# Performance work log

Hardware: AMD Instinct MI355X
Metric: run time of the kernel (lower is better)

## Reference

```python
import jax, jax.numpy as jnp
import numpy as np

NEWS_DIM = 400
HID = 200  # user_query_vector_dim
B, L0 = 512, 200
MIN_LOG = 2  # min_log_length=1 incremented by add_pad


def setup_inputs() -> dict:
    key = jax.random.key(0)
    k1, k2, k3, k4, k5 = jax.random.split(key, 5)
    log_vec = jax.random.normal(k1, (B, L0, NEWS_DIM), dtype=jnp.float32)
    log_mask = jnp.ones((B, L0), dtype=jnp.float32)
    pad_embedding = jax.random.normal(k2, (1, NEWS_DIM), dtype=jnp.float32)
    # att_fc1: Linear(news_dim -> hid), att_fc2: Linear(hid -> 1)
    W1 = jax.random.normal(k3, (HID, NEWS_DIM), dtype=jnp.float32) / np.sqrt(NEWS_DIM)
    b1 = jnp.zeros((HID,), dtype=jnp.float32)
    W2 = jax.random.normal(k4, (1, HID), dtype=jnp.float32) / np.sqrt(HID)
    b2 = jnp.zeros((1,), dtype=jnp.float32)
    return {"log_vec": log_vec, "log_mask": log_mask, "pad_embedding": pad_embedding,
            "W1": W1, "b1": b1, "W2": W2, "b2": b2}


def reference(log_vec, log_mask, pad_embedding, W1, b1, W2, b2):
    Bz, _, D = log_vec.shape
    # add_pad: prepend pad doc, then drop last -> (B, L, D) with L = L0
    pad = jnp.broadcast_to(pad_embedding, (Bz, 1, D))
    vec = jnp.concatenate([pad, log_vec], axis=1)[:, :-1, :]
    L = vec.shape[1]
    G = L + 1 - MIN_LOG  # = L0 - 1
    # autor_mask = ones(L,G).triu(1-MIN_LOG).T -> (G, L)
    tri = jnp.triu(jnp.ones((L, G), dtype=jnp.float32), k=1 - MIN_LOG).T
    # use_pad=False: multiply in history mask (broadcast over L)
    auto_mask = tri[None, :, :] * log_mask[:, :-1, None]  # (B, G, L)
    # score MLP computed once per (B, L); identical across G so broadcast
    s = (jnp.tanh(jnp.einsum('bld,hd->blh', vec, W1) + b1) @ W2.T + b2)[..., 0]  # (B, L)
    w = jnp.where(auto_mask == 0, jnp.float32(-1e8), s[:, None, :])  # (B, G, L)
    w = jax.nn.softmax(w, axis=-1)
    user_vec = jnp.einsum('bgl,bld->bgd', w, vec)  # (B, G, D)
    return user_vec
```

## Files before the change

kernel.cpp:

```cpp
#include <hip/hip_runtime.h>
#include <math.h>


#define BATCH 512
#define LHIST 200
#define DNEWS 400
#define HID   200
#define GOUT  199

#define NKO   50
#define KOSTR 224
#define NNT   7

typedef __attribute__((ext_vector_type(8)))  _Float16 f16x8;
typedef __attribute__((ext_vector_type(4)))  _Float16 f16x4;
typedef __attribute__((ext_vector_type(4)))  ushort   u16x4;
typedef __attribute__((ext_vector_type(2)))  _Float16 h2;
typedef __attribute__((ext_vector_type(2)))  __fp16   h2raw;
typedef __attribute__((ext_vector_type(16))) float    f32x16;

__device__ __forceinline__ h2 pkrtz(float a, float b) {
    union { h2raw r; h2 h; } u;
    u.r = __builtin_amdgcn_cvt_pkrtz(a, b);
    return u.h;
}

__device__ __forceinline__ float ftanh(float x) {
    x = fminf(fmaxf(x, -15.f), 15.f);
    const float t = __expf(2.f * x);
    return (t - 1.f) * __builtin_amdgcn_rcpf(t + 1.f);
}

__global__ __launch_bounds__(256)
void w1cvt_kernel(const float* __restrict__ W1, _Float16* __restrict__ Wc)
{
    const int q = blockIdx.x * 256 + threadIdx.x;
    if (q >= NKO * KOSTR * 4) return;
    const int j2 = q & 3;
    const int c  = q >> 2;
    const int n  = c % KOSTR;
    const int ko = c / KOSTR;
    float a = 0.f, b = 0.f;
    if (n < HID) {
        const float2 v = *(const float2*)(W1 + (size_t)n * DNEWS + ko * 8 + j2 * 2);
        a = v.x; b = v.y;
    }
    *(h2*)(Wc + (size_t)c * 8 + j2 * 2) = pkrtz(a, b);
}

__global__ __launch_bounds__(512, 1)
void fused_kernel(const float* __restrict__ log_vec,
                  const float* __restrict__ pad_emb,
                  const _Float16* __restrict__ Wc,
                  const float* __restrict__ b1,
                  const float* __restrict__ W2,
                  const float* __restrict__ b2,
                  float* __restrict__ out)
{
    __shared__ _Float16 V[LHIST * DNEWS];
    __shared__ float    s_lds[224];
    __shared__ float    e_lds[LHIST];
    __shared__ float    iz_lds[LHIST];

    const int tid  = threadIdx.x;
    const int w    = tid >> 6;
    const int lane = tid & 63;
    const int col  = lane & 31;
    const int hi   = lane >> 5;
    const int b    = blockIdx.x;

    const float* base = log_vec + (size_t)b * LHIST * DNEWS;

#pragma unroll
    for (int it = 0; it < 40; ++it) {
        const int idx = it * 512 + tid;
        if (idx < LHIST * 100) {
            const int row = idx / 100;
            const int q   = idx - row * 100;
            const float* src = (row == 0) ? (pad_emb + q * 4)
                                          : (base + (size_t)(row - 1) * DNEWS + q * 4);
            const float4 v = *(const float4*)src;
            union { u16x4 u; h2 h[2]; } cv;
            cv.h[0] = pkrtz(v.x, v.y);
            cv.h[1] = pkrtz(v.z, v.w);
            *(u16x4*)&V[row * DNEWS + q * 4] = cv.u;
        }
    }
    __syncthreads();

    if (w < 7) {
        const int arow = min(w * 32 + col, LHIST - 1);
        f32x16 acc[NNT];
#pragma unroll
        for (int nt = 0; nt < NNT; ++nt)
#pragma unroll
            for (int r = 0; r < 16; ++r) acc[nt][r] = 0.f;

#pragma unroll
        for (int ks = 0; ks < 25; ++ks) {
            const int ko = ks * 2 + hi;
            const f16x8 av = *(const f16x8*)&V[arow * DNEWS + ko * 8];
#pragma unroll
            for (int nt = 0; nt < NNT; ++nt) {
                const int n = nt * 32 + col;
                const f16x8 bv = *(const f16x8*)&Wc[((size_t)ko * KOSTR + n) * 8];
                acc[nt] = __builtin_amdgcn_mfma_f32_32x32x16_f16(av, bv, acc[nt], 0, 0, 0);
            }
        }

        float b1x[NNT], w2x[NNT];
#pragma unroll
        for (int nt = 0; nt < NNT; ++nt) {
            const int n = nt * 32 + col;
            const bool val = n < HID;
            b1x[nt] = val ? b1[n] : 0.f;
            w2x[nt] = val ? W2[n] : 0.f;
        }
        float p[16];
#pragma unroll
        for (int r = 0; r < 16; ++r) {
            float a = 0.f;
#pragma unroll
            for (int nt = 0; nt < NNT; ++nt)
                a += ftanh(acc[nt][r] + b1x[nt]) * w2x[nt];
            p[r] = a;
        }
#pragma unroll
        for (int r = 0; r < 16; ++r) {
#pragma unroll
            for (int off = 1; off < 32; off <<= 1)
                p[r] += __shfl_xor(p[r], off);
        }
        if (col == 0) {
            const float b2v = b2[0];
#pragma unroll
            for (int r = 0; r < 16; ++r)
                s_lds[w * 32 + (r & 3) + 8 * (r >> 2) + 4 * hi] = p[r] + b2v;
        }
    }
    __syncthreads();

    if (w == 0) {
        const bool act = lane < 50;
        float4 s4 = make_float4(0.f, 0.f, 0.f, 0.f);
        if (act) s4 = *(const float4*)&s_lds[lane * 4];
        float mx = act ? fmaxf(fmaxf(s4.x, s4.y), fmaxf(s4.z, s4.w)) : -INFINITY;
#pragma unroll
        for (int off = 32; off; off >>= 1) mx = fmaxf(mx, __shfl_xor(mx, off));

        float e0 = 0.f, e1 = 0.f, e2 = 0.f, e3 = 0.f;
        if (act) {
            e0 = __expf(s4.x - mx); e1 = __expf(s4.y - mx);
            e2 = __expf(s4.z - mx); e3 = __expf(s4.w - mx);
        }
        const float p0 = e0, p1 = p0 + e1, p2 = p1 + e2, p3 = p2 + e3;
        const float tot = p3;
        float run = tot;
#pragma unroll
        for (int off = 1; off < 64; off <<= 1) {
            const float v = __shfl_up(run, off);
            if (lane >= off) run += v;
        }
        const float bse = run - tot;
        if (act) {
            e_lds[lane*4+0] = e0;  e_lds[lane*4+1] = e1;
            e_lds[lane*4+2] = e2;  e_lds[lane*4+3] = e3;
            iz_lds[lane*4+0] = bse + p0;  iz_lds[lane*4+1] = bse + p1;
            iz_lds[lane*4+2] = bse + p2;  iz_lds[lane*4+3] = bse + p3;
        }
    }
    __syncthreads();
    if (tid < LHIST) iz_lds[tid] = 1.0f / iz_lds[tid];
    __syncthreads();

    {
        const int p    = w >> 1;
        const int half = w & 1;
        const int gs   = p * 50;
        const int ge   = (p == 3) ? GOUT : gs + 50;
        if (lane < 50) {
            const int d0 = half * 200 + lane * 4;
            float a0 = 0.f, a1 = 0.f, a2 = 0.f, a3 = 0.f;
            for (int l = 0; l <= gs; ++l) {
                const f16x4 vv = *(const f16x4*)&V[l * DNEWS + d0];
                const float el = e_lds[l];
                a0 += el * (float)vv[0];  a1 += el * (float)vv[1];
                a2 += el * (float)vv[2];  a3 += el * (float)vv[3];
            }
            float* orow = out + ((size_t)b * GOUT) * DNEWS + d0;
#pragma unroll 4
            for (int g = gs; g < ge; ++g) {
                const f16x4 vv = *(const f16x4*)&V[(g + 1) * DNEWS + d0];
                const float eg = e_lds[g + 1];
                const float iz = iz_lds[g + 1];
                a0 += eg * (float)vv[0];  a1 += eg * (float)vv[1];
                a2 += eg * (float)vv[2];  a3 += eg * (float)vv[3];
                float4 o;
                o.x = a0 * iz;  o.y = a1 * iz;  o.z = a2 * iz;  o.w = a3 * iz;
                *(float4*)(orow + (size_t)g * DNEWS) = o;
            }
        }
    }
}

extern "C" void kernel_launch(void* const* d_in, const int* in_sizes, int n_in,
                              void* d_out, int out_size, void* d_ws, size_t ws_size,
                              hipStream_t stream)
{
    const float* log_vec = (const float*)d_in[0];
    const float* pad_emb = (const float*)d_in[2];
    const float* W1 = (const float*)d_in[3];
    const float* b1 = (const float*)d_in[4];
    const float* W2 = (const float*)d_in[5];
    const float* b2 = (const float*)d_in[6];
    float* out = (float*)d_out;

    _Float16* Wc = (_Float16*)d_ws;

    hipLaunchKernelGGL(w1cvt_kernel, dim3((NKO * KOSTR * 4 + 255) / 256), dim3(256),
                       0, stream, W1, Wc);
    hipLaunchKernelGGL(fused_kernel, dim3(BATCH), dim3(512), 0, stream,
                       log_vec, pad_emb, Wc, b1, W2, b2, out);
}
```

Before: 113.6 us.

## Pipeline log_vec staging in row strips with per-strip MFMA and padded LDS

```diff
diff --git a/kernel.cpp b/kernel.cpp
--- a/kernel.cpp
+++ b/kernel.cpp
@@ -8,9 +8,11 @@
 #define HID   200
 #define GOUT  199
 
-#define NKO   50
-#define KOSTR 224
-#define NNT   7
+#define NKO    50
+#define KOSTR  224
+#define NNT    7
+#define NSTRIP 7
+#define VSTR   404
 
 typedef __attribute__((ext_vector_type(8)))  _Float16 f16x8;
 typedef __attribute__((ext_vector_type(4)))  _Float16 f16x4;
@@ -57,9 +59,8 @@
                   const float* __restrict__ b2,
                   float* __restrict__ out)
 {
-    __shared__ _Float16 V[LHIST * DNEWS];
-    __shared__ float    s_lds[224];
-    __shared__ float    e_lds[LHIST];
+    __shared__ _Float16 V[LHIST * VSTR];
+    __shared__ float    se_lds[LHIST];
     __shared__ float    iz_lds[LHIST];
 
     const int tid  = threadIdx.x;
@@ -71,79 +72,96 @@
 
     const float* base = log_vec + (size_t)b * LHIST * DNEWS;
 
-#pragma unroll
-    for (int it = 0; it < 40; ++it) {
-        const int idx = it * 512 + tid;
-        if (idx < LHIST * 100) {
-            const int row = idx / 100;
-            const int q   = idx - row * 100;
-            const float* src = (row == 0) ? (pad_emb + q * 4)
-                                          : (base + (size_t)(row - 1) * DNEWS + q * 4);
-            const float4 v = *(const float4*)src;
-            union { u16x4 u; h2 h[2]; } cv;
-            cv.h[0] = pkrtz(v.x, v.y);
-            cv.h[1] = pkrtz(v.z, v.w);
-            *(u16x4*)&V[row * DNEWS + q * 4] = cv.u;
-        }
-    }
+    const float b2v = b2[0];
+    if (tid < LHIST) se_lds[tid] = b2v;
+
+    const int  n    = w * 32 + col;
+    const bool nval = (w < NNT) && (n < HID);
+    const float b1x = nval ? b1[n] : 0.f;
+    const float w2x = nval ? W2[n] : 0.f;
+
+    float4 sreg[7];
+    auto stage_load = [&](int t) {
+#pragma unroll
+        for (int j = 0; j < 7; ++j) {
+            const int idx = j * 512 + tid;
+            if (idx < 3200) {
+                const int rl = idx / 100;
+                const int q  = idx - rl * 100;
+                const int R  = t * 32 + rl;
+                if (R < LHIST) {
+                    const float* src = (R == 0)
+                                         ? (pad_emb + q * 4)
+                                         : (base + (size_t)(R - 1) * DNEWS + q * 4);
+                    sreg[j] = *(const float4*)src;
+                }
+            }
+        }
+    };
+    auto stage_write = [&](int t) {
+#pragma unroll
+        for (int j = 0; j < 7; ++j) {
+            const int idx = j * 512 + tid;
+            if (idx < 3200) {
+                const int rl = idx / 100;
+                const int q  = idx - rl * 100;
+                const int R  = t * 32 + rl;
+                if (R < LHIST) {
+                    union { u16x4 u; h2 h[2]; } cv;
+                    cv.h[0] = pkrtz(sreg[j].x, sreg[j].y);
+                    cv.h[1] = pkrtz(sreg[j].z, sreg[j].w);
+                    *(u16x4*)&V[R * VSTR + q * 4] = cv.u;
+                }
+            }
+        }
+    };
+
+    stage_load(0);
+    stage_write(0);
     __syncthreads();
 
-    if (w < 7) {
-        const int arow = min(w * 32 + col, LHIST - 1);
-        f32x16 acc[NNT];
-#pragma unroll
-        for (int nt = 0; nt < NNT; ++nt)
-#pragma unroll
-            for (int r = 0; r < 16; ++r) acc[nt][r] = 0.f;
-
-#pragma unroll
-        for (int ks = 0; ks < 25; ++ks) {
-            const int ko = ks * 2 + hi;
-            const f16x8 av = *(const f16x8*)&V[arow * DNEWS + ko * 8];
-#pragma unroll
-            for (int nt = 0; nt < NNT; ++nt) {
-                const int n = nt * 32 + col;
+    for (int t = 0; t < NSTRIP; ++t) {
+        if (t + 1 < NSTRIP) stage_load(t + 1);
+        if (w < NNT) {
+            f32x16 acc;
+#pragma unroll
+            for (int r = 0; r < 16; ++r) acc[r] = 0.f;
+            const int arow = min(t * 32 + col, LHIST - 1);
+#pragma unroll
+            for (int ks = 0; ks < 25; ++ks) {
+                const int ko = ks * 2 + hi;
+                union { f16x8 v; f16x4 h[2]; } au;
+                au.h[0] = *(const f16x4*)&V[arow * VSTR + ko * 8];
+                au.h[1] = *(const f16x4*)&V[arow * VSTR + ko * 8 + 4];
                 const f16x8 bv = *(const f16x8*)&Wc[((size_t)ko * KOSTR + n) * 8];
-                acc[nt] = __builtin_amdgcn_mfma_f32_32x32x16_f16(av, bv, acc[nt], 0, 0, 0);
-            }
-        }
-
-        float b1x[NNT], w2x[NNT];
-#pragma unroll
-        for (int nt = 0; nt < NNT; ++nt) {
-            const int n = nt * 32 + col;
-            const bool val = n < HID;
-            b1x[nt] = val ? b1[n] : 0.f;
-            w2x[nt] = val ? W2[n] : 0.f;
-        }
-        float p[16];
-#pragma unroll
-        for (int r = 0; r < 16; ++r) {
-            float a = 0.f;
-#pragma unroll
-            for (int nt = 0; nt < NNT; ++nt)
-                a += ftanh(acc[nt][r] + b1x[nt]) * w2x[nt];
-            p[r] = a;
-        }
-#pragma unroll
-        for (int r = 0; r < 16; ++r) {
-#pragma unroll
-            for (int off = 1; off < 32; off <<= 1)
-                p[r] += __shfl_xor(p[r], off);
-        }
-        if (col == 0) {
-            const float b2v = b2[0];
+                acc = __builtin_amdgcn_mfma_f32_32x32x16_f16(au.v, bv, acc, 0, 0, 0);
+            }
+            float p[16];
 #pragma unroll
             for (int r = 0; r < 16; ++r)
-                s_lds[w * 32 + (r & 3) + 8 * (r >> 2) + 4 * hi] = p[r] + b2v;
-        }
-    }
-    __syncthreads();
+                p[r] = ftanh(acc[r] + b1x) * w2x;
+#pragma unroll
+            for (int r = 0; r < 16; ++r) {
+#pragma unroll
+                for (int off = 1; off < 32; off <<= 1)
+                    p[r] += __shfl_xor(p[r], off);
+            }
+            if (col == 0) {
+#pragma unroll
+                for (int r = 0; r < 16; ++r) {
+                    const int row = t * 32 + (r & 3) + 8 * (r >> 2) + 4 * hi;
+                    if (row < LHIST) atomicAdd(&se_lds[row], p[r]);
+                }
+            }
+        }
+        if (t + 1 < NSTRIP) stage_write(t + 1);
+        __syncthreads();
+    }
 
     if (w == 0) {
         const bool act = lane < 50;
         float4 s4 = make_float4(0.f, 0.f, 0.f, 0.f);
-        if (act) s4 = *(const float4*)&s_lds[lane * 4];
+        if (act) s4 = *(const float4*)&se_lds[lane * 4];
         float mx = act ? fmaxf(fmaxf(s4.x, s4.y), fmaxf(s4.z, s4.w)) : -INFINITY;
 #pragma unroll
         for (int off = 32; off; off >>= 1) mx = fmaxf(mx, __shfl_xor(mx, off));
@@ -163,8 +181,8 @@
         }
         const float bse = run - tot;
         if (act) {
-            e_lds[lane*4+0] = e0;  e_lds[lane*4+1] = e1;
-            e_lds[lane*4+2] = e2;  e_lds[lane*4+3] = e3;
+            se_lds[lane*4+0] = e0;  se_lds[lane*4+1] = e1;
+            se_lds[lane*4+2] = e2;  se_lds[lane*4+3] = e3;
             iz_lds[lane*4+0] = bse + p0;  iz_lds[lane*4+1] = bse + p1;
             iz_lds[lane*4+2] = bse + p2;  iz_lds[lane*4+3] = bse + p3;
         }
@@ -181,17 +199,18 @@
         if (lane < 50) {
             const int d0 = half * 200 + lane * 4;
             float a0 = 0.f, a1 = 0.f, a2 = 0.f, a3 = 0.f;
+#pragma unroll 4
             for (int l = 0; l <= gs; ++l) {
-                const f16x4 vv = *(const f16x4*)&V[l * DNEWS + d0];
-                const float el = e_lds[l];
+                const f16x4 vv = *(const f16x4*)&V[l * VSTR + d0];
+                const float el = se_lds[l];
                 a0 += el * (float)vv[0];  a1 += el * (float)vv[1];
                 a2 += el * (float)vv[2];  a3 += el * (float)vv[3];
             }
             float* orow = out + ((size_t)b * GOUT) * DNEWS + d0;
 #pragma unroll 4
             for (int g = gs; g < ge; ++g) {
-                const f16x4 vv = *(const f16x4*)&V[(g + 1) * DNEWS + d0];
-                const float eg = e_lds[g + 1];
+                const f16x4 vv = *(const f16x4*)&V[(g + 1) * VSTR + d0];
+                const float eg = se_lds[g + 1];
                 const float iz = iz_lds[g + 1];
                 a0 += eg * (float)vv[0];  a1 += eg * (float)vv[1];
                 a2 += eg * (float)vv[2];  a3 += eg * (float)vv[3];
```

New measurement: 117.8 us. 1.04x slower.

## Swap MFMA roles so waves own hidden columns; pad LDS rows; single-pass prefix output

Applied to the files above, without the earlier changes.

```diff
diff --git a/kernel.cpp b/kernel.cpp
--- a/kernel.cpp
+++ b/kernel.cpp
@@ -8,9 +8,11 @@
 #define HID   200
 #define GOUT  199
 
-#define NKO   50
-#define KOSTR 224
-#define NNT   7
+#define NKO    50
+#define KOSTR  224
+#define NNT    7
+#define NSTRIP 7
+#define VSTR   404
 
 typedef __attribute__((ext_vector_type(8)))  _Float16 f16x8;
 typedef __attribute__((ext_vector_type(4)))  _Float16 f16x4;
@@ -52,15 +54,14 @@
 void fused_kernel(const float* __restrict__ log_vec,
                   const float* __restrict__ pad_emb,
                   const _Float16* __restrict__ Wc,
-                  const float* __restrict__ b1,
+                  const float* __restrict__ b1v,
                   const float* __restrict__ W2,
                   const float* __restrict__ b2,
                   float* __restrict__ out)
 {
-    __shared__ _Float16 V[LHIST * DNEWS];
-    __shared__ float    s_lds[224];
-    __shared__ float    e_lds[LHIST];
-    __shared__ float    iz_lds[LHIST];
+    __shared__ _Float16 V[LHIST * VSTR];
+    __shared__ float    se[LHIST];
+    __shared__ float    iz[LHIST];
 
     const int tid  = threadIdx.x;
     const int w    = tid >> 6;
@@ -69,73 +70,74 @@
     const int hi   = lane >> 5;
     const int b    = blockIdx.x;
 
-    const float* base = log_vec + (size_t)b * LHIST * DNEWS;
-
-#pragma unroll
-    for (int it = 0; it < 40; ++it) {
-        const int idx = it * 512 + tid;
-        if (idx < LHIST * 100) {
-            const int row = idx / 100;
-            const int q   = idx - row * 100;
-            const float* src = (row == 0) ? (pad_emb + q * 4)
-                                          : (base + (size_t)(row - 1) * DNEWS + q * 4);
-            const float4 v = *(const float4*)src;
-            union { u16x4 u; h2 h[2]; } cv;
-            cv.h[0] = pkrtz(v.x, v.y);
-            cv.h[1] = pkrtz(v.z, v.w);
-            *(u16x4*)&V[row * DNEWS + q * 4] = cv.u;
-        }
-    }
-    __syncthreads();
-
-    if (w < 7) {
-        const int arow = min(w * 32 + col, LHIST - 1);
-        f32x16 acc[NNT];
-#pragma unroll
-        for (int nt = 0; nt < NNT; ++nt)
-#pragma unroll
-            for (int r = 0; r < 16; ++r) acc[nt][r] = 0.f;
+    if (tid < LHIST) se[tid] = b2[0];
+
+    {
+        const float* base = log_vec + (size_t)b * LHIST * DNEWS;
+#pragma unroll
+        for (int it = 0; it < 40; ++it) {
+            const int idx = it * 512 + tid;
+            if (idx < LHIST * 100) {
+                const int row = idx / 100;
+                const int q   = idx - row * 100;
+                const float* src = (row == 0)
+                                     ? (pad_emb + q * 4)
+                                     : (base + (size_t)(row - 1) * DNEWS + q * 4);
+                const float4 v = *(const float4*)src;
+                union { u16x4 u; h2 h[2]; } cv;
+                cv.h[0] = pkrtz(v.x, v.y);
+                cv.h[1] = pkrtz(v.z, v.w);
+                *(u16x4*)&V[row * VSTR + q * 4] = cv.u;
+            }
+        }
+    }
+    __syncthreads();
+
+    if (w < NNT) {
+        const int  n    = w * 32 + col;
+        const bool nval = n < HID;
+        const float b1x = nval ? b1v[n] : 0.f;
+        const float w2x = nval ? W2[n]  : 0.f;
+
+        f32x16 acc[NSTRIP];
+#pragma unroll
+        for (int t = 0; t < NSTRIP; ++t)
+#pragma unroll
+            for (int r = 0; r < 16; ++r) acc[t][r] = 0.f;
 
 #pragma unroll
         for (int ks = 0; ks < 25; ++ks) {
             const int ko = ks * 2 + hi;
-            const f16x8 av = *(const f16x8*)&V[arow * DNEWS + ko * 8];
-#pragma unroll
-            for (int nt = 0; nt < NNT; ++nt) {
-                const int n = nt * 32 + col;
-                const f16x8 bv = *(const f16x8*)&Wc[((size_t)ko * KOSTR + n) * 8];
-                acc[nt] = __builtin_amdgcn_mfma_f32_32x32x16_f16(av, bv, acc[nt], 0, 0, 0);
-            }
-        }
-
-        float b1x[NNT], w2x[NNT];
-#pragma unroll
-        for (int nt = 0; nt < NNT; ++nt) {
-            const int n = nt * 32 + col;
-            const bool val = n < HID;
-            b1x[nt] = val ? b1[n] : 0.f;
-            w2x[nt] = val ? W2[n] : 0.f;
-        }
-        float p[16];
-#pragma unroll
-        for (int r = 0; r < 16; ++r) {
-            float a = 0.f;
-#pragma unroll
-            for (int nt = 0; nt < NNT; ++nt)
-                a += ftanh(acc[nt][r] + b1x[nt]) * w2x[nt];
-            p[r] = a;
-        }
-#pragma unroll
-        for (int r = 0; r < 16; ++r) {
-#pragma unroll
-            for (int off = 1; off < 32; off <<= 1)
-                p[r] += __shfl_xor(p[r], off);
-        }
-        if (col == 0) {
-            const float b2v = b2[0];
+            const f16x8 bv = *(const f16x8*)&Wc[((size_t)ko * KOSTR + n) * 8];
+#pragma unroll
+            for (int t = 0; t < NSTRIP; ++t) {
+                const int arow = min(t * 32 + col, LHIST - 1);
+                union { f16x8 v; f16x4 h[2]; } au;
+                au.h[0] = *(const f16x4*)&V[arow * VSTR + ko * 8];
+                au.h[1] = *(const f16x4*)&V[arow * VSTR + ko * 8 + 4];
+                acc[t] = __builtin_amdgcn_mfma_f32_32x32x16_f16(au.v, bv, acc[t], 0, 0, 0);
+            }
+        }
+
+#pragma unroll
+        for (int t = 0; t < NSTRIP; ++t) {
+            float p[16];
 #pragma unroll
             for (int r = 0; r < 16; ++r)
-                s_lds[w * 32 + (r & 3) + 8 * (r >> 2) + 4 * hi] = p[r] + b2v;
+                p[r] = ftanh(acc[t][r] + b1x) * w2x;
+#pragma unroll
+            for (int r = 0; r < 16; ++r) {
+#pragma unroll
+                for (int off = 1; off < 32; off <<= 1)
+                    p[r] += __shfl_xor(p[r], off);
+            }
+            if (col == 0) {
+#pragma unroll
+                for (int r = 0; r < 16; ++r) {
+                    const int row = t * 32 + (r & 3) + 8 * (r >> 2) + 4 * hi;
+                    if (row < LHIST) atomicAdd(&se[row], p[r]);
+                }
+            }
         }
     }
     __syncthreads();
@@ -143,11 +145,10 @@
     if (w == 0) {
         const bool act = lane < 50;
         float4 s4 = make_float4(0.f, 0.f, 0.f, 0.f);
-        if (act) s4 = *(const float4*)&s_lds[lane * 4];
+        if (act) s4 = *(const float4*)&se[lane * 4];
         float mx = act ? fmaxf(fmaxf(s4.x, s4.y), fmaxf(s4.z, s4.w)) : -INFINITY;
 #pragma unroll
         for (int off = 32; off; off >>= 1) mx = fmaxf(mx, __shfl_xor(mx, off));
-
         float e0 = 0.f, e1 = 0.f, e2 = 0.f, e3 = 0.f;
         if (act) {
             e0 = __expf(s4.x - mx); e1 = __expf(s4.y - mx);
@@ -163,42 +164,33 @@
         }
         const float bse = run - tot;
         if (act) {
-            e_lds[lane*4+0] = e0;  e_lds[lane*4+1] = e1;
-            e_lds[lane*4+2] = e2;  e_lds[lane*4+3] = e3;
-            iz_lds[lane*4+0] = bse + p0;  iz_lds[lane*4+1] = bse + p1;
-            iz_lds[lane*4+2] = bse + p2;  iz_lds[lane*4+3] = bse + p3;
-        }
-    }
-    __syncthreads();
-    if (tid < LHIST) iz_lds[tid] = 1.0f / iz_lds[tid];
-    __syncthreads();
-
-    {
-        const int p    = w >> 1;
-        const int half = w & 1;
-        const int gs   = p * 50;
-        const int ge   = (p == 3) ? GOUT : gs + 50;
-        if (lane < 50) {
-            const int d0 = half * 200 + lane * 4;
-            float a0 = 0.f, a1 = 0.f, a2 = 0.f, a3 = 0.f;
-            for (int l = 0; l <= gs; ++l) {
-                const f16x4 vv = *(const f16x4*)&V[l * DNEWS + d0];
-                const float el = e_lds[l];
-                a0 += el * (float)vv[0];  a1 += el * (float)vv[1];
-                a2 += el * (float)vv[2];  a3 += el * (float)vv[3];
-            }
-            float* orow = out + ((size_t)b * GOUT) * DNEWS + d0;
-#pragma unroll 4
-            for (int g = gs; g < ge; ++g) {
-                const f16x4 vv = *(const f16x4*)&V[(g + 1) * DNEWS + d0];
-                const float eg = e_lds[g + 1];
-                const float iz = iz_lds[g + 1];
-                a0 += eg * (float)vv[0];  a1 += eg * (float)vv[1];
-                a2 += eg * (float)vv[2];  a3 += eg * (float)vv[3];
-                float4 o;
-                o.x = a0 * iz;  o.y = a1 * iz;  o.z = a2 * iz;  o.w = a3 * iz;
-                *(float4*)(orow + (size_t)g * DNEWS) = o;
-            }
+            se[lane*4+0] = e0;  se[lane*4+1] = e1;
+            se[lane*4+2] = e2;  se[lane*4+3] = e3;
+            iz[lane*4+0] = bse + p0;  iz[lane*4+1] = bse + p1;
+            iz[lane*4+2] = bse + p2;  iz[lane*4+3] = bse + p3;
+        }
+    }
+    __syncthreads();
+    if (tid < LHIST) iz[tid] = 1.0f / iz[tid];
+    __syncthreads();
+
+    if (tid < 100) {
+        const int d0 = tid * 4;
+        const f16x4 v0 = *(const f16x4*)&V[d0];
+        const float e0v = se[0];
+        float A0 = e0v * (float)v0[0], A1 = e0v * (float)v0[1];
+        float A2 = e0v * (float)v0[2], A3 = e0v * (float)v0[3];
+        float* ob = out + (size_t)b * GOUT * DNEWS + d0;
+#pragma unroll 8
+        for (int g = 0; g < GOUT; ++g) {
+            const f16x4 vv = *(const f16x4*)&V[(g + 1) * VSTR + d0];
+            const float e = se[g + 1];
+            const float z = iz[g + 1];
+            A0 += e * (float)vv[0];  A1 += e * (float)vv[1];
+            A2 += e * (float)vv[2];  A3 += e * (float)vv[3];
+            float4 o;
+            o.x = A0 * z;  o.y = A1 * z;  o.z = A2 * z;  o.w = A3 * z;
+            *(float4*)(ob + (size_t)g * DNEWS) = o;
         }
     }
 }
```

Result: slower. 120.1 us (+5.7%).
